# Performance work log

Hardware: AMD Instinct MI355X
Metric: run time of the kernel (lower is better)

Reference implementation:

```python
import jax, jax.numpy as jnp
import numpy as np

H = 16; DH = 64; D = H * DH
MEM = 1000            # config.memory_size
KT = 8 + 2            # k_similar + k_contiguous
THRESH = 0.5          # surprise_threshold


def _episodic_scan(k_flat):
    """k_flat: [B,S,D] per-token flattened keys. Sequentially (matching the torch
    per-sample python loop) segment each sequence by surprise, write segment-mean
    events into a FIFO memory, and retrieve top-KT events by cosine similarity
    against the last key. Ragged segments handled via masking (jit-safe)."""
    B, S, _ = k_flat.shape
    mem0 = jnp.zeros((MEM, D), k_flat.dtype)
    mv0 = jnp.zeros((MEM,), bool)

    def body(carry, kf):  # kf: [S,D]
        mem, mv = carry
        # surprise_t = ||k_t - k_{t-1}||, surprise_0 = 0
        diffs = jnp.linalg.norm(kf[1:] - kf[:-1], axis=-1)
        surprise = jnp.concatenate([jnp.zeros((1,), kf.dtype), diffs])
        thr = surprise.mean() + THRESH * jnp.std(surprise, ddof=1)  # torch.std is unbiased
        b = (surprise > thr).at[-1].set(True)  # boundary mask; last index forced
        bi = b.astype(jnp.int32)
        seg = jnp.cumsum(bi) - bi              # exclusive cumsum -> segment id per token
        sums = jax.ops.segment_sum(kf, seg, num_segments=S)
        cnts = jax.ops.segment_sum(jnp.ones((S,), kf.dtype), seg, num_segments=S)
        means = sums / jnp.maximum(cnts, 1.0)[:, None]  # [S,D] segment means (masked ragged)
        newv = jnp.arange(S) < bi.sum()
        # compact valid new events to the front (stable sort preserves order)
        o = jnp.argsort(jnp.logical_not(newv).astype(jnp.int32))
        comb = jnp.concatenate([mem, means[o]], axis=0)        # [MEM+S, D]
        cv = jnp.concatenate([mv, newv[o]], axis=0)
        # FIFO truncation: keep the last MEM valid events
        rank = jnp.cumsum(cv.astype(jnp.int32))
        keep = cv & (rank > rank[-1] - MEM)
        o2 = jnp.argsort(jnp.logical_not(keep).astype(jnp.int32))[:MEM]
        mem, mv = comb[o2], keep[o2]
        # retrieval: cosine similarity of last token's key vs memory, top-KT
        qf = kf[-1]
        qn = jnp.maximum(jnp.linalg.norm(qf), 1e-8)
        mn = jnp.maximum(jnp.linalg.norm(mem, axis=1), 1e-8)
        sims = jnp.where(mv, (mem @ qf) / (mn * qn), -jnp.inf)
        _, idx = jax.lax.top_k(sims, KT)
        return (mem, mv), mem[idx]  # retrieved events [KT, D]

    _, rets = jax.lax.scan(body, (mem0, mv0), k_flat)
    return rets  # [B, KT, D]


def setup_inputs() -> dict:
    key = jax.random.key(0)
    ks = jax.random.split(key, 6)
    B, S = 2, 2048
    return {
        "inputs": jax.random.normal(ks[0], (B, S, D), jnp.float32),
        "attention_mask": jnp.ones((B, S), jnp.int32),
        "Wq": jax.random.normal(ks[1], (D, D), jnp.float32) * 0.02,
        "Wk": jax.random.normal(ks[2], (D, D), jnp.float32) * 0.02,
        "Wv": jax.random.normal(ks[3], (D, D), jnp.float32) * 0.02,
        "Wo": jax.random.normal(ks[4], (D, D), jnp.float32) * 0.02,
    }


def reference(inputs, attention_mask, Wq, Wk, Wv, Wo):
    B, S, _ = inputs.shape
    qf = inputs @ Wq.T  # [B,S,D], per-token layout == keys.transpose(0,1).reshape(S,-1)
    kf = inputs @ Wk.T
    vf = inputs @ Wv.T
    q = qf.reshape(B, S, H, DH).transpose(0, 2, 1, 3)  # [B,H,S,DH]
    k = kf.reshape(B, S, H, DH).transpose(0, 2, 1, 3)
    v = vf.reshape(B, S, H, DH).transpose(0, 2, 1, 3)

    ret = _episodic_scan(kf)                               # [B,KT,D]
    ret_k = ret.reshape(B, KT, H, DH).transpose(0, 2, 1, 3)  # [B,H,KT,DH]
    aug_k = jnp.concatenate([ret_k, k], axis=2)            # [B,H,KT+S,DH]
    aug_v = jnp.concatenate([ret_k, v], axis=2)            # retrieved_v == retrieved_k

    scores = jnp.einsum("bhqd,bhkd->bhqk", q, aug_k) / jnp.sqrt(jnp.float32(DH))
    # ALiBi biases: zero for memory tokens, slopes*(pos_i-pos_j) for real tokens
    pos = jnp.arange(S, dtype=jnp.float32)
    pd = pos[:, None] - pos[None, :]                       # [S,S]
    slopes = 2.0 ** (-8.0 * jnp.arange(1, H + 1, dtype=jnp.float32) / H)
    bias_orig = slopes[None, :, None, None] * pd[None, None]  # [1,H,S,S]
    bias = jnp.concatenate(
        [jnp.zeros((1, H, S, KT), scores.dtype),
         jnp.broadcast_to(bias_orig, (1, H, S, S))], axis=3)
    scores = scores - bias
    # causal over real tokens; memory tokens always visible; attention_mask padded with 1s
    causal = jnp.concatenate(
        [jnp.ones((S, KT), bool), jnp.tril(jnp.ones((S, S), bool))], axis=1)
    aug_mask = jnp.concatenate(
        [jnp.ones((B, KT), jnp.int32), attention_mask], axis=1)
    visible = causal[None, None] & (aug_mask[:, None, None, :] > 0)
    scores = jnp.where(visible, scores, -jnp.inf)
    w = jax.nn.softmax(scores, axis=-1)
    out = jnp.einsum("bhqk,bhkd->bhqd", w, aug_v)
    out = out.transpose(0, 2, 1, 3).reshape(B, S, D)
    return out @ Wo.T
```

## Files before the change

### kernel.cpp

```cpp
#include <hip/hip_runtime.h>
#include <math.h>

#define B_ 2
#define S_ 2048
#define H_ 16
#define DH_ 64
#define D_ 1024
#define MEM_ 1000
#define KT_ 10
#define THRESH_ 0.5
#define BS_ (B_ * S_)
#define EVCAP_ (2 * S_)

typedef float f32x4 __attribute__((ext_vector_type(4)));
typedef short bf16x8 __attribute__((ext_vector_type(8)));
typedef short s16x4 __attribute__((ext_vector_type(4)));

__device__ inline unsigned short f2bf(float f) {
    union { float f; unsigned u; } v; v.f = f;
    unsigned u = v.u;
    unsigned r = (u + 0x7FFFu + ((u >> 16) & 1u)) >> 16;
    return (unsigned short)r;
}
__device__ inline float bf2f(unsigned short h) {
    union { unsigned u; float f; } v; v.u = ((unsigned)h) << 16; return v.f;
}

__device__ __forceinline__ void gload16(const short* gp, const short* lp) {
    __builtin_amdgcn_global_load_lds(
        (__attribute__((address_space(1))) void*)(unsigned long long)gp,
        (__attribute__((address_space(3))) void*)(unsigned)(unsigned long long)lp,
        16, 0, 0);
}

struct SpArgs {
    const float* X;
    short *Xh, *Xm, *Xl;
    const float* W[4];
    short *Wh[4], *Wm[4], *Wl[4];
    int nx4;
};
__global__ __launch_bounds__(256) void split_all_kernel(SpArgs sa)
{
    int bid = blockIdx.x;
    const float* src; short *ph, *pm, *pl; int i;
    if (bid < 4096) {
        i = bid * 256 + threadIdx.x;
        if (i >= sa.nx4) return;
        src = sa.X; ph = sa.Xh; pm = sa.Xm; pl = sa.Xl;
    } else {
        int wb = bid - 4096;
        int y = wb >> 10;
        i = (wb & 1023) * 256 + threadIdx.x;
        src = sa.W[y]; ph = sa.Wh[y]; pm = sa.Wm[y]; pl = sa.Wl[y];
    }
    float4 x = ((const float4*)src)[i];
    float xs[4] = {x.x, x.y, x.z, x.w};
    s16x4 hv, mv, lv;
    bool wl = (pl != nullptr);
#pragma unroll
    for (int j = 0; j < 4; ++j) {
        unsigned short hb = f2bf(xs[j]);
        float hf = bf2f(hb);
        float r1 = xs[j] - hf;
        unsigned short mb = f2bf(r1);
        hv[j] = (short)hb; mv[j] = (short)mb;
        if (wl) {
            float mf = bf2f(mb);
            lv[j] = (short)f2bf(r1 - mf);
        }
    }
    ((s16x4*)ph)[i] = hv;
    ((s16x4*)pm)[i] = mv;
    if (wl) ((s16x4*)pl)[i] = lv;
}

struct G8Args {
    const short* A[4][3];
    const short* B[4][3];
    short* outb[4];
    float* outf[4];
    int gsbase[4];
    int nt;
};

__global__ __launch_bounds__(512, 2) void gemm8(G8Args ga)
{
    __shared__ __align__(16) short Abuf[3][2][4096];
    __shared__ __align__(16) short Bbuf[3][2][4096];

    int wg = blockIdx.x;
    int lin = (wg & 7) * 32 + (wg >> 3);
    int jb = lin >> 4;
    int by = lin & 15;
    int g = jb >> 2;
    int bcol = jb & 3;

    int tid = threadIdx.x;
    int w = tid >> 6, l = tid & 63;
    int wm = w >> 2, wn = w & 3;
    int lg = l >> 4, lc = l & 15;

    const short* A0 = ga.A[g][0]; const short* A1 = ga.A[g][1]; const short* A2 = ga.A[g][2];
    const short* B0 = ga.B[g][0]; const short* B1 = ga.B[g][1]; const short* B2 = ga.B[g][2];
    const int gs0 = ga.gsbase[g];
    const int NT = ga.nt;

    const int u = tid;
    const int vswz = (u & 7) ^ ((u >> 3) & 7);
    const int srow = 2 * (u >> 3) + (vswz >> 2);
    const int skcol = (vswz & 3) * 8;
    const size_t abase = (size_t)(by * 256) * D_ + skcol;
    const size_t bbase = (size_t)(bcol * 256) * D_ + skcol;
    const int dst0 = w * 512;

    auto STAGE_A = [&](int ts, int d) {
        int tt = ts >> 5; int k0 = (ts & 31) << 5;
        const short* At = (tt == 0) ? A0 : ((tt == 1) ? A1 : A2);
        const short* Ab = At + abase + k0;
#pragma unroll
        for (int h = 0; h < 2; ++h)
            gload16(Ab + (size_t)(h * 128 + srow) * D_, &Abuf[d][h][dst0]);
    };
    auto STAGE_B = [&](int ts, int d) {
        int tt = ts >> 5; int k0 = (ts & 31) << 5;
        const short* Bt = (tt == 0) ? B0 : ((tt == 1) ? B1 : B2);
        const short* Bb = Bt + bbase + k0;
#pragma unroll
        for (int h = 0; h < 2; ++h)
            gload16(Bb + (size_t)(h * 128 + srow) * D_, &Bbuf[d][h][dst0]);
    };

    f32x4 acc[8][4] = {};
    const int psa = (((((lc & 1) << 2) | lg)) ^ ((lc >> 1) & 7)) * 8;
    const int rbase = (lc >> 1) * 64;

    STAGE_A(gs0, 0); STAGE_B(gs0, 0);
    STAGE_A(gs0 + 1, 1); STAGE_B(gs0 + 1, 1);
    asm volatile("s_waitcnt vmcnt(4)" ::: "memory");
    asm volatile("s_barrier" ::: "memory");
    __builtin_amdgcn_sched_barrier(0);

    int d = 0, ds = 2;
    for (int t = 0; t < NT; ++t) {
        const short* Ab0 = &Abuf[d][wm][rbase + psa];
        const short* Bb0 = &Bbuf[d][wn >> 1][(wn & 1) * 2048 + rbase + psa];
        bf16x8 bv[4], av[4];
#pragma unroll
        for (int nf = 0; nf < 4; ++nf) bv[nf] = *(const bf16x8*)&Bb0[nf * 512];
#pragma unroll
        for (int mf = 0; mf < 4; ++mf) av[mf] = *(const bf16x8*)&Ab0[mf * 512];
        if (t + 2 < NT) STAGE_A(gs0 + t + 2, ds);
        asm volatile("s_barrier" ::: "memory");
        asm volatile("s_waitcnt lgkmcnt(0)" ::: "memory");
        __builtin_amdgcn_sched_barrier(0);
        __builtin_amdgcn_s_setprio(1);
#pragma unroll
        for (int mf = 0; mf < 4; ++mf)
#pragma unroll
            for (int nf = 0; nf < 4; ++nf)
                acc[mf][nf] = __builtin_amdgcn_mfma_f32_16x16x32_bf16(av[mf], bv[nf], acc[mf][nf], 0, 0, 0);
        __builtin_amdgcn_s_setprio(0);
        asm volatile("s_barrier" ::: "memory");
#pragma unroll
        for (int mf = 0; mf < 4; ++mf) av[mf] = *(const bf16x8*)&Ab0[(4 + mf) * 512];
        if (t + 2 < NT) STAGE_B(gs0 + t + 2, ds);
        asm volatile("s_barrier" ::: "memory");
        asm volatile("s_waitcnt lgkmcnt(0)" ::: "memory");
        __builtin_amdgcn_sched_barrier(0);
        __builtin_amdgcn_s_setprio(1);
#pragma unroll
        for (int mf = 0; mf < 4; ++mf)
#pragma unroll
            for (int nf = 0; nf < 4; ++nf)
                acc[4 + mf][nf] = __builtin_amdgcn_mfma_f32_16x16x32_bf16(av[mf], bv[nf], acc[4 + mf][nf], 0, 0, 0);
        __builtin_amdgcn_s_setprio(0);
        if (t + 2 < NT) asm volatile("s_waitcnt vmcnt(4)" ::: "memory");
        else            asm volatile("s_waitcnt vmcnt(0)" ::: "memory");
        asm volatile("s_barrier" ::: "memory");
        __builtin_amdgcn_sched_barrier(0);
        d = (d == 2) ? 0 : d + 1;
        ds = (ds == 2) ? 0 : ds + 1;
    }

    short* ob = ga.outb[g];
    if (ob) {
#pragma unroll
        for (int mf = 0; mf < 8; ++mf)
#pragma unroll
            for (int nf = 0; nf < 4; ++nf)
#pragma unroll
                for (int reg = 0; reg < 4; ++reg) {
                    int row = by * 256 + wm * 128 + mf * 16 + lg * 4 + reg;
                    int col = bcol * 256 + wn * 64 + nf * 16 + lc;
                    ob[(size_t)row * D_ + col] = (short)f2bf(acc[mf][nf][reg]);
                }
    } else {
        float* of = ga.outf[g];
#pragma unroll
        for (int mf = 0; mf < 8; ++mf)
#pragma unroll
            for (int nf = 0; nf < 4; ++nf)
#pragma unroll
                for (int reg = 0; reg < 4; ++reg) {
                    int row = by * 256 + wm * 128 + mf * 16 + lg * 4 + reg;
                    int col = bcol * 256 + wn * 64 + nf * 16 + lc;
                    of[(size_t)row * D_ + col] = acc[mf][nf][reg];
                }
    }
}

__global__ __launch_bounds__(256) void fixup_kernel(const short* __restrict__ vbf,
                                                    short* __restrict__ vbfT,
                                                    float* __restrict__ kf,
                                                    const float* __restrict__ kp1,
                                                    short* __restrict__ kbf)
{
    int bid = blockIdx.x;
    int tid = threadIdx.x;
    if (bid < 1024) {
        __shared__ short st[64][70];
        int t = bid;
        int s0 = (t & 31) * 64;
        int h = (t >> 5) & 15;
        int b = t >> 9;
        int r = tid >> 2, cb = (tid & 3) * 16;
        const short* src = vbf + (size_t)(b * S_ + s0 + r) * D_ + h * DH_ + cb;
        *(bf16x8*)&st[r][cb] = *(const bf16x8*)src;
        *(bf16x8*)&st[r][cb + 8] = *(const bf16x8*)(src + 8);
        __syncthreads();
        int c = tid >> 2, sb = (tid & 3) * 16;
        short tmp[16];
#pragma unroll
        for (int i = 0; i < 16; ++i) tmp[i] = st[sb + i][c];
        short* dst = vbfT + ((size_t)(b * H_ + h) * DH_ + c) * S_ + s0 + sb;
        *(bf16x8*)dst = *(bf16x8*)&tmp[0];
        *(bf16x8*)(dst + 8) = *(bf16x8*)&tmp[8];
    } else {
        size_t i = (size_t)(bid - 1024) * 256 + tid;
        float4 a = ((const float4*)kf)[i];
        float4 b = ((const float4*)kp1)[i];
        float4 s = {a.x + b.x, a.y + b.y, a.z + b.z, a.w + b.w};
        ((float4*)kf)[i] = s;
        s16x4 o;
        o[0] = (short)f2bf(s.x); o[1] = (short)f2bf(s.y);
        o[2] = (short)f2bf(s.z); o[3] = (short)f2bf(s.w);
        ((s16x4*)kbf)[i] = o;
    }
}

__global__ __launch_bounds__(256) void addo4_kernel(const float* __restrict__ p0,
                                                    const float* __restrict__ p1,
                                                    const float* __restrict__ p2,
                                                    const float* __restrict__ p3,
                                                    float* __restrict__ out)
{
    size_t i = (size_t)blockIdx.x * 256 + threadIdx.x;
    float4 a = ((const float4*)p0)[i];
    float4 b = ((const float4*)p1)[i];
    float4 c = ((const float4*)p2)[i];
    float4 d = ((const float4*)p3)[i];
    float4 s = {((a.x + b.x) + c.x) + d.x, ((a.y + b.y) + c.y) + d.y,
                ((a.z + b.z) + c.z) + d.z, ((a.w + b.w) + c.w) + d.w};
    ((float4*)out)[i] = s;
}

__global__ __launch_bounds__(256) void surprise_kernel(const float* __restrict__ kf,
                                                       double* __restrict__ sur)
{
    int t = blockIdx.x;
    int b = blockIdx.y;
    if (t == 0) { if (threadIdx.x == 0) sur[(size_t)b * S_] = 0.0; return; }
    const float* kfb = kf + (size_t)b * S_ * D_;
    __shared__ double red[256];
    double acc = 0.0;
    for (int d = threadIdx.x; d < D_; d += 256) {
        double df = (double)kfb[(size_t)t * D_ + d] - (double)kfb[(size_t)(t - 1) * D_ + d];
        acc += df * df;
    }
    red[threadIdx.x] = acc;
    __syncthreads();
    for (int s = 128; s > 0; s >>= 1) {
        if (threadIdx.x < s) red[threadIdx.x] += red[threadIdx.x + s];
        __syncthreads();
    }
    if (threadIdx.x == 0) sur[(size_t)b * S_ + t] = sqrt(red[0]);
}

__global__ __launch_bounds__(256) void boundary2_kernel(const double* __restrict__ sur,
                                                        int* __restrict__ seg_start,
                                                        int* __restrict__ seg_end,
                                                        int* __restrict__ scal)
{
    __shared__ double lsur[S_];
    __shared__ double red[256];
    __shared__ double sh_mean, sh_thr;
    __shared__ int cnt[256];
    int tid = threadIdx.x;
    int running = 0;
    for (int b = 0; b < B_; ++b) {
        __syncthreads();
        for (int t = tid; t < S_; t += 256) lsur[t] = sur[(size_t)b * S_ + t];
        __syncthreads();
        double a = 0.0;
        for (int t = tid; t < S_; t += 256) a += lsur[t];
        red[tid] = a;
        __syncthreads();
        for (int s = 128; s > 0; s >>= 1) {
            if (tid < s) red[tid] += red[tid + s];
            __syncthreads();
        }
        if (tid == 0) sh_mean = red[0] / (double)S_;
        __syncthreads();
        double mean = sh_mean;
        a = 0.0;
        for (int t = tid; t < S_; t += 256) { double d = lsur[t] - mean; a += d * d; }
        red[tid] = a;
        __syncthreads();
        for (int s = 128; s > 0; s >>= 1) {
            if (tid < s) red[tid] += red[tid + s];
            __syncthreads();
        }
        if (tid == 0) sh_thr = mean + THRESH_ * sqrt(red[0] / (double)(S_ - 1));
        __syncthreads();
        double thr = sh_thr;
        bool flg[8];
        int c = 0;
#pragma unroll
        for (int j = 0; j < 8; ++j) {
            int t = tid * 8 + j;
            flg[j] = (lsur[t] > thr) || (t == S_ - 1);
            c += flg[j] ? 1 : 0;
        }
        cnt[tid] = c;
        __syncthreads();
        for (int off = 1; off < 256; off <<= 1) {
            int v = cnt[tid];
            int add = (tid >= off) ? cnt[tid - off] : 0;
            __syncthreads();
            cnt[tid] = v + add;
            __syncthreads();
        }
        int r = (tid == 0) ? 0 : cnt[tid - 1];
        int* se = seg_end + b * S_;
        int* ss = seg_start + b * S_;
#pragma unroll
        for (int j = 0; j < 8; ++j) {
            if (flg[j]) { se[r] = tid * 8 + j; ++r; }
        }
        __syncthreads();
        int n = cnt[255];
        for (int i = tid; i < n; i += 256)
            ss[i] = (i == 0) ? 0 : se[i - 1] + 1;
        if (tid == 0) {
            scal[4 + b] = n;
            scal[6 + b] = running;
        }
        running += n;
        __syncthreads();
    }
}

__global__ __launch_bounds__(256) void seg_means_kernel(const float* __restrict__ kf,
                                                        float* __restrict__ events,
                                                        const int* __restrict__ seg_start,
                                                        const int* __restrict__ seg_end,
                                                        const int* __restrict__ scal)
{
    int g = blockIdx.x;
    int b = blockIdx.y;
    if (g >= scal[4 + b]) return;
    const float* kfb = kf + (size_t)b * S_ * D_;
    int s = seg_start[b * S_ + g], e = seg_end[b * S_ + g];
    double inv = 1.0 / (double)(e - s + 1);
    size_t obase = (size_t)(scal[6 + b] + g) * D_;
    for (int d = threadIdx.x; d < D_; d += 256) {
        double acc = 0.0;
        for (int r = s; r <= e; ++r) acc += (double)kfb[(size_t)r * D_ + d];
        events[obase + d] = (float)(acc * inv);
    }
}

__global__ __launch_bounds__(256) void sims_kernel(const float* __restrict__ events,
                                                   const float* __restrict__ kf,
                                                   float* __restrict__ sims,
                                                   const int* __restrict__ scal)
{
    int e = blockIdx.x;
    int b = blockIdx.y;
    int total = scal[6 + b] + scal[4 + b];
    int w = total < MEM_ ? total : MEM_;
    float* sb = sims + b * MEM_;
    if (e >= w) { if (threadIdx.x == 0) sb[e] = -INFINITY; return; }
    int wstart = total - w;
    const float* ev = events + (size_t)(wstart + e) * D_;
    const float* q = kf + ((size_t)(b * S_ + S_ - 1)) * D_;
    __shared__ double r1[256], r2[256], r3[256];
    int tid = threadIdx.x;
    double dot = 0.0, n2 = 0.0, q2 = 0.0;
    for (int d = tid; d < D_; d += 256) {
        double ed = ev[d], qd = q[d];
        dot += ed * qd; n2 += ed * ed; q2 += qd * qd;
    }
    r1[tid] = dot; r2[tid] = n2; r3[tid] = q2;
    __syncthreads();
    for (int s = 128; s > 0; s >>= 1) {
        if (tid < s) { r1[tid] += r1[tid + s]; r2[tid] += r2[tid + s]; r3[tid] += r3[tid + s]; }
        __syncthreads();
    }
    if (tid == 0) {
        double mn = sqrt(r2[0]); if (mn < 1e-8) mn = 1e-8;
        double qn = sqrt(r3[0]); if (qn < 1e-8) qn = 1e-8;
        sb[e] = (float)(r1[0] / (mn * qn));
    }
}

__global__ __launch_bounds__(256) void topk_kernel(const float* __restrict__ events,
                                                   float* __restrict__ sims,
                                                   float* __restrict__ ret,
                                                   const int* __restrict__ scal)
{
    int b = blockIdx.x;
    int total = scal[6 + b] + scal[4 + b];
    int w = total < MEM_ ? total : MEM_;
    int wstart = total - w;
    float* sb = sims + b * MEM_;
    float* retb = ret + (size_t)b * KT_ * D_;
    __shared__ float bv[256];
    __shared__ int bidx[256];
    __shared__ int chosen;
    int tid = threadIdx.x;
    for (int r = 0; r < KT_; ++r) {
        float best = -INFINITY;
        int bi = 0x7fffffff;
        for (int e = tid; e < w; e += 256) {
            float v = sb[e];
            if (v > best || (v == best && e < bi)) { best = v; bi = e; }
        }
        bv[tid] = best; bidx[tid] = bi;
        __syncthreads();
        for (int s = 128; s > 0; s >>= 1) {
            if (tid < s) {
                if (bv[tid + s] > bv[tid] || (bv[tid + s] == bv[tid] && bidx[tid + s] < bidx[tid])) {
                    bv[tid] = bv[tid + s]; bidx[tid] = bidx[tid + s];
                }
            }
            __syncthreads();
        }
        if (tid == 0) {
            chosen = (r < w) ? bidx[0] : -1;
            if (chosen >= 0) sb[chosen] = -INFINITY;
        }
        __syncthreads();
        int c = chosen;
        if (c >= 0) {
            const float* ev = events + (size_t)(wstart + c) * D_;
            for (int d = tid; d < D_; d += 256) retb[(size_t)r * D_ + d] = ev[d];
        } else {
            for (int d = tid; d < D_; d += 256) retb[(size_t)r * D_ + d] = 0.0f;
        }
        __syncthreads();
    }
}

#define QTT 128
#define KTT 128
__global__ __launch_bounds__(512, 4) void attn_mfma_kernel(const short* __restrict__ qbf,
                                                           const short* __restrict__ kbf,
                                                           const short* __restrict__ vbfT,
                                                           const float* __restrict__ ret,
                                                           const int* __restrict__ amask,
                                                           short* __restrict__ AOh,
                                                           short* __restrict__ AOm)
{
    __shared__ __align__(16) short k_s[KTT][72];
    __shared__ __align__(16) short vT_s[DH_][136];
    __shared__ __align__(16) short p_s[8][16][136];

    const float LOG2E = 1.4426950408889634f;
    int bid = blockIdx.x;
    int xcd = bid & 7;
    int idx = bid >> 3;
    int qtslot = idx >> 2;
    int hbL = idx & 3;
    int qt = (qtslot < 8) ? (15 - qtslot) : (qtslot - 8);
    int hb = xcd * 4 + hbL;
    int h = hb & 15, b = hb >> 4;
    int q0 = qt * QTT;

    int tid = threadIdx.x;
    int w = tid >> 6, l = tid & 63;
    int lg = l >> 4, lc = l & 15;
    int qb = q0 + w * 16;
    float scale2 = 0.125f * LOG2E;
    float slope2 = exp2f(-0.5f * (float)(h + 1)) * LOG2E;

    bf16x8 qfr[2];
#pragma unroll
    for (int half = 0; half < 2; ++half)
        qfr[half] = *(const bf16x8*)(qbf + ((size_t)(b * S_ + qb + lc)) * D_ + h * DH_ + half * 32 + lg * 8);

    float mrow[4], lrow[4], fac[4];
#pragma unroll
    for (int r = 0; r < 4; ++r) { mrow[r] = -INFINITY; lrow[r] = 0.0f; }
    f32x4 O[4] = {};

    int skr = tid >> 2;
    int skc = (tid & 3) * 16;
    int sdv = tid >> 3;
    int skk = (tid & 7) * 16;

    const short* kptr = kbf + ((size_t)(b * S_ + skr)) * D_ + h * DH_ + skc;
    const short* vptr = vbfT + ((size_t)(b * H_ + h) * DH_ + sdv) * S_ + skk;

    int ntiles = qt + 1;
    bf16x8 kr0 = *(const bf16x8*)kptr, kr1 = *(const bf16x8*)(kptr + 8);
    bf16x8 vr0 = *(const bf16x8*)vptr, vr1 = *(const bf16x8*)(vptr + 8);

    for (int tile = 0; tile < ntiles; ++tile) {
        int j0 = tile * KTT;
        __syncthreads();
        *(bf16x8*)&k_s[skr][skc] = kr0;
        *(bf16x8*)&k_s[skr][skc + 8] = kr1;
        *(bf16x8*)&vT_s[sdv][skk] = vr0;
        *(bf16x8*)&vT_s[sdv][skk + 8] = vr1;
        __syncthreads();
        if (tile + 1 < ntiles) {
            const short* kp = kptr + (size_t)(tile + 1) * KTT * D_;
            kr0 = *(const bf16x8*)kp; kr1 = *(const bf16x8*)(kp + 8);
            const short* vp = vptr + (tile + 1) * KTT;
            vr0 = *(const bf16x8*)vp; vr1 = *(const bf16x8*)(vp + 8);
        }

        float sc[8][4];
        int am[8];
#pragma unroll
        for (int kt = 0; kt < 8; ++kt) am[kt] = amask[b * S_ + j0 + kt * 16 + lc];
        bool fullvis = (j0 + (KTT - 1) <= qb);
#pragma unroll
        for (int kt = 0; kt < 8; ++kt) {
            f32x4 s = {0.0f, 0.0f, 0.0f, 0.0f};
            bf16x8 k0 = *(const bf16x8*)&k_s[kt * 16 + lc][lg * 8];
            bf16x8 k1 = *(const bf16x8*)&k_s[kt * 16 + lc][32 + lg * 8];
            s = __builtin_amdgcn_mfma_f32_16x16x32_bf16(qfr[0], k0, s, 0, 0, 0);
            s = __builtin_amdgcn_mfma_f32_16x16x32_bf16(qfr[1], k1, s, 0, 0, 0);
            int jg = j0 + kt * 16 + lc;
            if (fullvis) {
#pragma unroll
                for (int reg = 0; reg < 4; ++reg) {
                    int qi = qb + lg * 4 + reg;
                    sc[kt][reg] = (am[kt] > 0) ? (s[reg] * scale2 - slope2 * (float)(qi - jg)) : -INFINITY;
                }
            } else {
#pragma unroll
                for (int reg = 0; reg < 4; ++reg) {
                    int qi = qb + lg * 4 + reg;
                    bool vis = (jg <= qi) && (am[kt] > 0);
                    sc[kt][reg] = vis ? (s[reg] * scale2 - slope2 * (float)(qi - jg)) : -INFINITY;
                }
            }
        }

#pragma unroll
        for (int reg = 0; reg < 4; ++reg) {
            float tm = fmaxf(fmaxf(fmaxf(sc[0][reg], sc[1][reg]), fmaxf(sc[2][reg], sc[3][reg])),
                             fmaxf(fmaxf(sc[4][reg], sc[5][reg]), fmaxf(sc[6][reg], sc[7][reg])));
#pragma unroll
            for (int msk = 1; msk <= 8; msk <<= 1) tm = fmaxf(tm, __shfl_xor(tm, msk));
            float mnew = fmaxf(mrow[reg], tm);
            fac[reg] = exp2f(mrow[reg] - mnew);
            mrow[reg] = mnew;
            float rs = 0.0f;
#pragma unroll
            for (int kt = 0; kt < 8; ++kt) {
                float p = exp2f(sc[kt][reg] - mnew);
                sc[kt][reg] = p;
                rs += p;
            }
#pragma unroll
            for (int msk = 1; msk <= 8; msk <<= 1) rs += __shfl_xor(rs, msk);
            lrow[reg] = lrow[reg] * fac[reg] + rs;
        }

        int parity = l & 1;
#pragma unroll
        for (int kt = 0; kt < 8; ++kt) {
#pragma unroll
            for (int rp = 0; rp < 4; rp += 2) {
                float s0 = sc[kt][rp];
                float s1 = sc[kt][rp + 1];
                float o0 = __shfl_xor(s0, 1);
                float o1 = __shfl_xor(s1, 1);
                float lo, hi; int reg;
                if (parity == 0) { lo = s0; hi = o0; reg = rp; }
                else             { lo = o1; hi = s1; reg = rp + 1; }
                unsigned pk = (unsigned)f2bf(lo) | ((unsigned)f2bf(hi) << 16);
                *(unsigned*)&p_s[w][lg * 4 + reg][kt * 16 + (lc & ~1)] = pk;
            }
        }
        __syncthreads();

#pragma unroll
        for (int db = 0; db < 4; ++db) {
#pragma unroll
            for (int reg = 0; reg < 4; ++reg) O[db][reg] *= fac[reg];
        }
#pragma unroll
        for (int kh = 0; kh < 4; ++kh) {
            bf16x8 a = *(const bf16x8*)&p_s[w][lc][kh * 32 + lg * 8];
#pragma unroll
            for (int db = 0; db < 4; ++db) {
                bf16x8 vb = *(const bf16x8*)&vT_s[db * 16 + lc][kh * 32 + lg * 8];
                O[db] = __builtin_amdgcn_mfma_f32_16x16x32_bf16(a, vb, O[db], 0, 0, 0);
            }
        }
    }

    {
        int sr = tid >> 3;
        int sc0 = (tid & 7) * 8;
        __syncthreads();
        short kv[8];
        if (sr < KT_) {
            const float* rp = ret + ((size_t)(b * KT_ + sr)) * D_ + h * DH_ + sc0;
            float4 a0 = *(const float4*)rp;
            float4 a1 = *(const float4*)(rp + 4);
            kv[0] = (short)f2bf(a0.x); kv[1] = (short)f2bf(a0.y);
            kv[2] = (short)f2bf(a0.z); kv[3] = (short)f2bf(a0.w);
            kv[4] = (short)f2bf(a1.x); kv[5] = (short)f2bf(a1.y);
            kv[6] = (short)f2bf(a1.z); kv[7] = (short)f2bf(a1.w);
        } else {
#pragma unroll
            for (int i = 0; i < 8; ++i) kv[i] = 0;
        }
        *(bf16x8*)&k_s[sr][sc0] = *(bf16x8*)&kv[0];
        __syncthreads();
        short tv[8];
#pragma unroll
        for (int i = 0; i < 8; ++i) {
            int key = sc0 + i;
            tv[i] = (key < KT_) ? k_s[key][sr] : (short)0;
        }
        *(bf16x8*)&vT_s[sr][sc0] = *(bf16x8*)&tv[0];

        float scm[4];
        {
            f32x4 s = {0.0f, 0.0f, 0.0f, 0.0f};
            bf16x8 k0 = *(const bf16x8*)&k_s[lc][lg * 8];
            bf16x8 k1 = *(const bf16x8*)&k_s[lc][32 + lg * 8];
            s = __builtin_amdgcn_mfma_f32_16x16x32_bf16(qfr[0], k0, s, 0, 0, 0);
            s = __builtin_amdgcn_mfma_f32_16x16x32_bf16(qfr[1], k1, s, 0, 0, 0);
#pragma unroll
            for (int reg = 0; reg < 4; ++reg)
                scm[reg] = (lc < KT_) ? s[reg] * scale2 : -INFINITY;
        }
        float pm[4];
#pragma unroll
        for (int reg = 0; reg < 4; ++reg) {
            float tm = scm[reg];
#pragma unroll
            for (int msk = 1; msk <= 8; msk <<= 1) tm = fmaxf(tm, __shfl_xor(tm, msk));
            float mnew = fmaxf(mrow[reg], tm);
            fac[reg] = exp2f(mrow[reg] - mnew);
            mrow[reg] = mnew;
            float p = exp2f(scm[reg] - mnew);
            pm[reg] = p;
            float rs = p;
#pragma unroll
            for (int msk = 1; msk <= 8; msk <<= 1) rs += __shfl_xor(rs, msk);
            lrow[reg] = lrow[reg] * fac[reg] + rs;
        }
        int parity = l & 1;
#pragma unroll
        for (int kt = 0; kt < 2; ++kt) {
#pragma unroll
            for (int rp = 0; rp < 4; rp += 2) {
                float s0 = (kt == 1) ? 0.0f : pm[rp];
                float s1 = (kt == 1) ? 0.0f : pm[rp + 1];
                float o0 = __shfl_xor(s0, 1);
                float o1 = __shfl_xor(s1, 1);
                float lo, hi; int reg;
                if (parity == 0) { lo = s0; hi = o0; reg = rp; }
                else             { lo = o1; hi = s1; reg = rp + 1; }
                unsigned pk = (unsigned)f2bf(lo) | ((unsigned)f2bf(hi) << 16);
                *(unsigned*)&p_s[w][lg * 4 + reg][kt * 16 + (lc & ~1)] = pk;
            }
        }
        __syncthreads();
#pragma unroll
        for (int db = 0; db < 4; ++db) {
#pragma unroll
            for (int reg = 0; reg < 4; ++reg) O[db][reg] *= fac[reg];
        }
        {
            bf16x8 a = *(const bf16x8*)&p_s[w][lc][lg * 8];
#pragma unroll
            for (int db = 0; db < 4; ++db) {
                bf16x8 vb = *(const bf16x8*)&vT_s[db * 16 + lc][lg * 8];
                O[db] = __builtin_amdgcn_mfma_f32_16x16x32_bf16(a, vb, O[db], 0, 0, 0);
            }
        }
    }

#pragma unroll
    for (int db = 0; db < 4; ++db) {
#pragma unroll
        for (int reg = 0; reg < 4; ++reg) {
            int qi = qb + lg * 4 + reg;
            size_t idx2 = ((size_t)(b * S_ + qi)) * D_ + h * DH_ + db * 16 + lc;
            float o = O[db][reg] / lrow[reg];
            unsigned short hb2 = f2bf(o);
            float hf = bf2f(hb2);
            unsigned short mb = f2bf(o - hf);
            AOh[idx2] = (short)hb2;
            AOm[idx2] = (short)mb;
        }
    }
}

extern "C" void kernel_launch(void* const* d_in, const int* in_sizes, int n_in,
                              void* d_out, int out_size, void* d_ws, size_t ws_size,
                              hipStream_t stream)
{
    const float* X = (const float*)d_in[0];
    const int* amask = (const int*)d_in[1];
    const float* Wq = (const float*)d_in[2];
    const float* Wk = (const float*)d_in[3];
    const float* Wv = (const float*)d_in[4];
    const float* Wo = (const float*)d_in[5];
    float* out = (float*)d_out;

    char* p = (char*)d_ws;
    auto alloc = [&](size_t bytes) -> char* {
        char* r = p; p += (bytes + 255) & ~(size_t)255; return r;
    };
    double* sur = (double*)alloc((size_t)B_ * S_ * sizeof(double));
    float* kacc = (float*)alloc((size_t)2 * BS_ * D_ * sizeof(float));
    float* events = (float*)alloc((size_t)EVCAP_ * D_ * sizeof(float));
    float* ret = (float*)alloc((size_t)B_ * KT_ * D_ * sizeof(float));
    float* sims = (float*)alloc((size_t)B_ * MEM_ * sizeof(float));
    int* seg_start = (int*)alloc((size_t)B_ * S_ * sizeof(int));
    int* seg_end = (int*)alloc((size_t)B_ * S_ * sizeof(int));
    int* scal = (int*)alloc(64);
    short* qbf = (short*)alloc((size_t)BS_ * D_ * sizeof(short));
    short* vbf = (short*)alloc((size_t)BS_ * D_ * sizeof(short));
    short* vbfT = (short*)alloc((size_t)B_ * H_ * DH_ * S_ * sizeof(short));
    short* Xh = (short*)alloc((size_t)BS_ * D_ * sizeof(short));
    short* Xm = (short*)alloc((size_t)BS_ * D_ * sizeof(short));
    short* Xl = (short*)alloc((size_t)BS_ * D_ * sizeof(short));
    short* Wqh = (short*)alloc((size_t)D_ * D_ * sizeof(short));
    short* Wqm = (short*)alloc((size_t)D_ * D_ * sizeof(short));
    short* Wvh = (short*)alloc((size_t)D_ * D_ * sizeof(short));
    short* Wvm = (short*)alloc((size_t)D_ * D_ * sizeof(short));
    short* Woh = (short*)alloc((size_t)D_ * D_ * sizeof(short));
    short* Wom = (short*)alloc((size_t)D_ * D_ * sizeof(short));
    short* Wkh = (short*)alloc((size_t)D_ * D_ * sizeof(short));
    short* Wkm = (short*)alloc((size_t)D_ * D_ * sizeof(short));
    short* Wkl = (short*)alloc((size_t)D_ * D_ * sizeof(short));
    if ((size_t)(p - (char*)d_ws) > ws_size) return;

    float* kf = kacc;
    float* kp1 = kacc + (size_t)BS_ * D_;
    short* kbf = Xl;

    {
        SpArgs sa = {};
        sa.X = X; sa.Xh = Xh; sa.Xm = Xm; sa.Xl = Xl;
        sa.W[0] = Wq; sa.Wh[0] = Wqh; sa.Wm[0] = Wqm; sa.Wl[0] = nullptr;
        sa.W[1] = Wk; sa.Wh[1] = Wkh; sa.Wm[1] = Wkm; sa.Wl[1] = Wkl;
        sa.W[2] = Wv; sa.Wh[2] = Wvh; sa.Wm[2] = Wvm; sa.Wl[2] = nullptr;
        sa.W[3] = Wo; sa.Wh[3] = Woh; sa.Wm[3] = Wom; sa.Wl[3] = nullptr;
        sa.nx4 = BS_ * D_ / 4;
        split_all_kernel<<<4096 + 4096, 256, 0, stream>>>(sa);
    }

    {
        G8Args ga = {};
        ga.A[0][0] = Xm;  ga.A[0][1] = Xh;  ga.A[0][2] = Xh;
        ga.B[0][0] = Wqh; ga.B[0][1] = Wqm; ga.B[0][2] = Wqh;
        ga.outb[0] = qbf;
        ga.A[1][0] = Xm;  ga.A[1][1] = Xh;  ga.A[1][2] = Xh;
        ga.B[1][0] = Wvh; ga.B[1][1] = Wvm; ga.B[1][2] = Wvh;
        ga.outb[1] = vbf;
        ga.A[2][0] = Xh;  ga.A[2][1] = Xm;  ga.A[2][2] = Xm;
        ga.B[2][0] = Wkm; ga.B[2][1] = Wkh; ga.B[2][2] = Wkm;
        ga.outf[2] = kf;
        ga.A[3][0] = Xh;  ga.A[3][1] = Xl;  ga.A[3][2] = Xh;
        ga.B[3][0] = Wkl; ga.B[3][1] = Wkh; ga.B[3][2] = Wkh;
        ga.outf[3] = kp1;
        ga.gsbase[0] = 0; ga.gsbase[1] = 0; ga.gsbase[2] = 0; ga.gsbase[3] = 0;
        ga.nt = 96;
        gemm8<<<256, 512, 0, stream>>>(ga);
    }
    fixup_kernel<<<1024 + BS_ * D_ / 4 / 256, 256, 0, stream>>>(vbf, vbfT, kf, kp1, kbf);

    surprise_kernel<<<dim3(S_, B_), 256, 0, stream>>>(kf, sur);
    boundary2_kernel<<<1, 256, 0, stream>>>(sur, seg_start, seg_end, scal);
    seg_means_kernel<<<dim3(S_, B_), 256, 0, stream>>>(kf, events, seg_start, seg_end, scal);
    sims_kernel<<<dim3(MEM_, B_), 256, 0, stream>>>(events, kf, sims, scal);
    topk_kernel<<<B_, 256, 0, stream>>>(events, sims, ret, scal);

    attn_mfma_kernel<<<512, 512, 0, stream>>>(qbf, kbf, vbfT, ret, amask, Xh, Xm);

    {
        float* p2 = events;
        float* p3 = (float*)qbf;
        G8Args ga = {};
        for (int g = 0; g < 4; ++g) {
            ga.A[g][0] = Xm;  ga.A[g][1] = Xh;  ga.A[g][2] = Xh;
            ga.B[g][0] = Woh; ga.B[g][1] = Wom; ga.B[g][2] = Woh;
            ga.gsbase[g] = g * 24;
        }
        ga.outf[0] = kf; ga.outf[1] = kp1; ga.outf[2] = p2; ga.outf[3] = p3;
        ga.nt = 24;
        gemm8<<<256, 512, 0, stream>>>(ga);
        addo4_kernel<<<BS_ * D_ / 4 / 256, 256, 0, stream>>>(kf, kp1, p2, p3, out);
    }
}
```

Before: 344.9 us.

## Fuse episodic scan stages into one cooperative kernel and simplify GEMM inner loop

Replaces the five separate scan kernels (surprise, boundary, segment means, similarity, top-k) with one cooperative kernel of 1024 blocks that uses grid-wide syncs between phases. The goal is to remove the launch gaps between these small, serial kernels. Separately, the GEMM main loop now loads all eight A fragments at once, issues both A and B staging loads together, and drops the intermediate barriers and waitcnts. The GEMM change increases register pressure and may introduce LDS hazards, because the next-stage loads are no longer fenced by barriers after the fragment reads.

```diff
diff --git a/kernel.cpp b/kernel.cpp
--- a/kernel.cpp
+++ b/kernel.cpp
@@ -1,5 +1,8 @@
 #include <hip/hip_runtime.h>
+#include <hip/hip_cooperative_groups.h>
 #include <math.h>
+
+namespace cg = cooperative_groups;
 
 #define B_ 2
 #define S_ 2048
@@ -145,35 +148,18 @@
     for (int t = 0; t < NT; ++t) {
         const short* Ab0 = &Abuf[d][wm][rbase + psa];
         const short* Bb0 = &Bbuf[d][wn >> 1][(wn & 1) * 2048 + rbase + psa];
-        bf16x8 bv[4], av[4];
+        bf16x8 av[8], bv[4];
 #pragma unroll
         for (int nf = 0; nf < 4; ++nf) bv[nf] = *(const bf16x8*)&Bb0[nf * 512];
 #pragma unroll
-        for (int mf = 0; mf < 4; ++mf) av[mf] = *(const bf16x8*)&Ab0[mf * 512];
-        if (t + 2 < NT) STAGE_A(gs0 + t + 2, ds);
-        asm volatile("s_barrier" ::: "memory");
-        asm volatile("s_waitcnt lgkmcnt(0)" ::: "memory");
-        __builtin_amdgcn_sched_barrier(0);
+        for (int mf = 0; mf < 8; ++mf) av[mf] = *(const bf16x8*)&Ab0[mf * 512];
+        if (t + 2 < NT) { STAGE_A(gs0 + t + 2, ds); STAGE_B(gs0 + t + 2, ds); }
         __builtin_amdgcn_s_setprio(1);
 #pragma unroll
-        for (int mf = 0; mf < 4; ++mf)
+        for (int mf = 0; mf < 8; ++mf)
 #pragma unroll
             for (int nf = 0; nf < 4; ++nf)
                 acc[mf][nf] = __builtin_amdgcn_mfma_f32_16x16x32_bf16(av[mf], bv[nf], acc[mf][nf], 0, 0, 0);
-        __builtin_amdgcn_s_setprio(0);
-        asm volatile("s_barrier" ::: "memory");
-#pragma unroll
-        for (int mf = 0; mf < 4; ++mf) av[mf] = *(const bf16x8*)&Ab0[(4 + mf) * 512];
-        if (t + 2 < NT) STAGE_B(gs0 + t + 2, ds);
-        asm volatile("s_barrier" ::: "memory");
-        asm volatile("s_waitcnt lgkmcnt(0)" ::: "memory");
-        __builtin_amdgcn_sched_barrier(0);
-        __builtin_amdgcn_s_setprio(1);
-#pragma unroll
-        for (int mf = 0; mf < 4; ++mf)
-#pragma unroll
-            for (int nf = 0; nf < 4; ++nf)
-                acc[4 + mf][nf] = __builtin_amdgcn_mfma_f32_16x16x32_bf16(av[mf], bv[nf], acc[4 + mf][nf], 0, 0, 0);
         __builtin_amdgcn_s_setprio(0);
         if (t + 2 < NT) asm volatile("s_waitcnt vmcnt(4)" ::: "memory");
         else            asm volatile("s_waitcnt vmcnt(0)" ::: "memory");
@@ -265,201 +251,203 @@
     ((float4*)out)[i] = s;
 }
 
-__global__ __launch_bounds__(256) void surprise_kernel(const float* __restrict__ kf,
-                                                       double* __restrict__ sur)
+struct ScanArgs {
+    const float* kf;
+    double* sur;
+    int* seg_start;
+    int* seg_end;
+    int* scal;
+    float* events;
+    float* sims;
+    float* ret;
+};
+
+__global__ __launch_bounds__(256) void scan_all_kernel(ScanArgs a)
 {
-    int t = blockIdx.x;
-    int b = blockIdx.y;
-    if (t == 0) { if (threadIdx.x == 0) sur[(size_t)b * S_] = 0.0; return; }
-    const float* kfb = kf + (size_t)b * S_ * D_;
+    cg::grid_group grid = cg::this_grid();
     __shared__ double red[256];
-    double acc = 0.0;
-    for (int d = threadIdx.x; d < D_; d += 256) {
-        double df = (double)kfb[(size_t)t * D_ + d] - (double)kfb[(size_t)(t - 1) * D_ + d];
-        acc += df * df;
-    }
-    red[threadIdx.x] = acc;
-    __syncthreads();
-    for (int s = 128; s > 0; s >>= 1) {
-        if (threadIdx.x < s) red[threadIdx.x] += red[threadIdx.x + s];
-        __syncthreads();
-    }
-    if (threadIdx.x == 0) sur[(size_t)b * S_ + t] = sqrt(red[0]);
-}
-
-__global__ __launch_bounds__(256) void boundary2_kernel(const double* __restrict__ sur,
-                                                        int* __restrict__ seg_start,
-                                                        int* __restrict__ seg_end,
-                                                        int* __restrict__ scal)
-{
+    __shared__ double r2[256], r3[256];
     __shared__ double lsur[S_];
-    __shared__ double red[256];
+    __shared__ int cnt[256];
     __shared__ double sh_mean, sh_thr;
-    __shared__ int cnt[256];
-    int tid = threadIdx.x;
-    int running = 0;
-    for (int b = 0; b < B_; ++b) {
-        __syncthreads();
-        for (int t = tid; t < S_; t += 256) lsur[t] = sur[(size_t)b * S_ + t];
-        __syncthreads();
-        double a = 0.0;
-        for (int t = tid; t < S_; t += 256) a += lsur[t];
-        red[tid] = a;
+    __shared__ float bvv[256];
+    __shared__ int bidx[256];
+    __shared__ int chosen;
+    int bid = blockIdx.x, tid = threadIdx.x;
+    int nb = gridDim.x;
+
+    for (int item = bid; item < B_ * S_; item += nb) {
+        int b = item >> 11, t = item & (S_ - 1);
+        if (t == 0) { if (tid == 0) a.sur[(size_t)b * S_] = 0.0; continue; }
+        const float* kfb = a.kf + (size_t)b * S_ * D_;
+        double acc = 0.0;
+        for (int d = tid; d < D_; d += 256) {
+            double df = (double)kfb[(size_t)t * D_ + d] - (double)kfb[(size_t)(t - 1) * D_ + d];
+            acc += df * df;
+        }
+        red[tid] = acc;
         __syncthreads();
         for (int s = 128; s > 0; s >>= 1) {
             if (tid < s) red[tid] += red[tid + s];
             __syncthreads();
         }
-        if (tid == 0) sh_mean = red[0] / (double)S_;
-        __syncthreads();
-        double mean = sh_mean;
-        a = 0.0;
-        for (int t = tid; t < S_; t += 256) { double d = lsur[t] - mean; a += d * d; }
-        red[tid] = a;
+        if (tid == 0) a.sur[(size_t)b * S_ + t] = sqrt(red[0]);
+        __syncthreads();
+    }
+    __threadfence();
+    grid.sync();
+
+    if (bid == 0) {
+        int running = 0;
+        for (int b = 0; b < B_; ++b) {
+            __syncthreads();
+            for (int t = tid; t < S_; t += 256) lsur[t] = a.sur[(size_t)b * S_ + t];
+            __syncthreads();
+            double s1 = 0.0;
+            for (int t = tid; t < S_; t += 256) s1 += lsur[t];
+            red[tid] = s1;
+            __syncthreads();
+            for (int s = 128; s > 0; s >>= 1) {
+                if (tid < s) red[tid] += red[tid + s];
+                __syncthreads();
+            }
+            if (tid == 0) sh_mean = red[0] / (double)S_;
+            __syncthreads();
+            double mean = sh_mean;
+            s1 = 0.0;
+            for (int t = tid; t < S_; t += 256) { double d = lsur[t] - mean; s1 += d * d; }
+            red[tid] = s1;
+            __syncthreads();
+            for (int s = 128; s > 0; s >>= 1) {
+                if (tid < s) red[tid] += red[tid + s];
+                __syncthreads();
+            }
+            if (tid == 0) sh_thr = mean + THRESH_ * sqrt(red[0] / (double)(S_ - 1));
+            __syncthreads();
+            double thr = sh_thr;
+            bool flg[8];
+            int c = 0;
+#pragma unroll
+            for (int j = 0; j < 8; ++j) {
+                int t = tid * 8 + j;
+                flg[j] = (lsur[t] > thr) || (t == S_ - 1);
+                c += flg[j] ? 1 : 0;
+            }
+            cnt[tid] = c;
+            __syncthreads();
+            for (int off = 1; off < 256; off <<= 1) {
+                int v = cnt[tid];
+                int add = (tid >= off) ? cnt[tid - off] : 0;
+                __syncthreads();
+                cnt[tid] = v + add;
+                __syncthreads();
+            }
+            int r = (tid == 0) ? 0 : cnt[tid - 1];
+            int* se = a.seg_end + b * S_;
+            int* ss = a.seg_start + b * S_;
+#pragma unroll
+            for (int j = 0; j < 8; ++j) {
+                if (flg[j]) { se[r] = tid * 8 + j; ++r; }
+            }
+            __syncthreads();
+            int n = cnt[255];
+            for (int i = tid; i < n; i += 256)
+                ss[i] = (i == 0) ? 0 : se[i - 1] + 1;
+            if (tid == 0) {
+                a.scal[4 + b] = n;
+                a.scal[6 + b] = running;
+            }
+            running += n;
+            __syncthreads();
+        }
+    }
+    __threadfence();
+    grid.sync();
+
+    for (int item = bid; item < B_ * S_; item += nb) {
+        int b = item >> 11, g = item & (S_ - 1);
+        if (g >= a.scal[4 + b]) continue;
+        const float* kfb = a.kf + (size_t)b * S_ * D_;
+        int s = a.seg_start[b * S_ + g], e = a.seg_end[b * S_ + g];
+        double inv = 1.0 / (double)(e - s + 1);
+        size_t obase = (size_t)(a.scal[6 + b] + g) * D_;
+        for (int d = tid; d < D_; d += 256) {
+            double acc = 0.0;
+            for (int r = s; r <= e; ++r) acc += (double)kfb[(size_t)r * D_ + d];
+            a.events[obase + d] = (float)(acc * inv);
+        }
+    }
+    __threadfence();
+    grid.sync();
+
+    for (int item = bid; item < B_ * MEM_; item += nb) {
+        int b = item / MEM_, e = item - b * MEM_;
+        int total = a.scal[6 + b] + a.scal[4 + b];
+        int w = total < MEM_ ? total : MEM_;
+        float* sb = a.sims + b * MEM_;
+        if (e >= w) { if (tid == 0) sb[e] = -INFINITY; continue; }
+        int wstart = total - w;
+        const float* ev = a.events + (size_t)(wstart + e) * D_;
+        const float* q = a.kf + ((size_t)(b * S_ + S_ - 1)) * D_;
+        double dot = 0.0, n2 = 0.0, q2 = 0.0;
+        for (int d = tid; d < D_; d += 256) {
+            double ed = ev[d], qd = q[d];
+            dot += ed * qd; n2 += ed * ed; q2 += qd * qd;
+        }
+        red[tid] = dot; r2[tid] = n2; r3[tid] = q2;
         __syncthreads();
         for (int s = 128; s > 0; s >>= 1) {
-            if (tid < s) red[tid] += red[tid + s];
-            __syncthreads();
-        }
-        if (tid == 0) sh_thr = mean + THRESH_ * sqrt(red[0] / (double)(S_ - 1));
-        __syncthreads();
-        double thr = sh_thr;
-        bool flg[8];
-        int c = 0;
-#pragma unroll
-        for (int j = 0; j < 8; ++j) {
-            int t = tid * 8 + j;
-            flg[j] = (lsur[t] > thr) || (t == S_ - 1);
-            c += flg[j] ? 1 : 0;
-        }
-        cnt[tid] = c;
-        __syncthreads();
-        for (int off = 1; off < 256; off <<= 1) {
-            int v = cnt[tid];
-            int add = (tid >= off) ? cnt[tid - off] : 0;
-            __syncthreads();
-            cnt[tid] = v + add;
-            __syncthreads();
-        }
-        int r = (tid == 0) ? 0 : cnt[tid - 1];
-        int* se = seg_end + b * S_;
-        int* ss = seg_start + b * S_;
-#pragma unroll
-        for (int j = 0; j < 8; ++j) {
-            if (flg[j]) { se[r] = tid * 8 + j; ++r; }
-        }
-        __syncthreads();
-        int n = cnt[255];
-        for (int i = tid; i < n; i += 256)
-            ss[i] = (i == 0) ? 0 : se[i - 1] + 1;
+            if (tid < s) { red[tid] += red[tid + s]; r2[tid] += r2[tid + s]; r3[tid] += r3[tid + s]; }
+            __syncthreads();
+        }
         if (tid == 0) {
-            scal[4 + b] = n;
-            scal[6 + b] = running;
-        }
-        running += n;
-        __syncthreads();
-    }
-}
-
-__global__ __launch_bounds__(256) void seg_means_kernel(const float* __restrict__ kf,
-                                                        float* __restrict__ events,
-                                                        const int* __restrict__ seg_start,
-                                                        const int* __restrict__ seg_end,
-                                                        const int* __restrict__ scal)
-{
-    int g = blockIdx.x;
-    int b = blockIdx.y;
-    if (g >= scal[4 + b]) return;
-    const float* kfb = kf + (size_t)b * S_ * D_;
-    int s = seg_start[b * S_ + g], e = seg_end[b * S_ + g];
-    double inv = 1.0 / (double)(e - s + 1);
-    size_t obase = (size_t)(scal[6 + b] + g) * D_;
-    for (int d = threadIdx.x; d < D_; d += 256) {
-        double acc = 0.0;
-        for (int r = s; r <= e; ++r) acc += (double)kfb[(size_t)r * D_ + d];
-        events[obase + d] = (float)(acc * inv);
-    }
-}
-
-__global__ __launch_bounds__(256) void sims_kernel(const float* __restrict__ events,
-                                                   const float* __restrict__ kf,
-                                                   float* __restrict__ sims,
-                                                   const int* __restrict__ scal)
-{
-    int e = blockIdx.x;
-    int b = blockIdx.y;
-    int total = scal[6 + b] + scal[4 + b];
-    int w = total < MEM_ ? total : MEM_;
-    float* sb = sims + b * MEM_;
-    if (e >= w) { if (threadIdx.x == 0) sb[e] = -INFINITY; return; }
-    int wstart = total - w;
-    const float* ev = events + (size_t)(wstart + e) * D_;
-    const float* q = kf + ((size_t)(b * S_ + S_ - 1)) * D_;
-    __shared__ double r1[256], r2[256], r3[256];
-    int tid = threadIdx.x;
-    double dot = 0.0, n2 = 0.0, q2 = 0.0;
-    for (int d = tid; d < D_; d += 256) {
-        double ed = ev[d], qd = q[d];
-        dot += ed * qd; n2 += ed * ed; q2 += qd * qd;
-    }
-    r1[tid] = dot; r2[tid] = n2; r3[tid] = q2;
-    __syncthreads();
-    for (int s = 128; s > 0; s >>= 1) {
-        if (tid < s) { r1[tid] += r1[tid + s]; r2[tid] += r2[tid + s]; r3[tid] += r3[tid + s]; }
-        __syncthreads();
-    }
-    if (tid == 0) {
-        double mn = sqrt(r2[0]); if (mn < 1e-8) mn = 1e-8;
-        double qn = sqrt(r3[0]); if (qn < 1e-8) qn = 1e-8;
-        sb[e] = (float)(r1[0] / (mn * qn));
-    }
-}
-
-__global__ __launch_bounds__(256) void topk_kernel(const float* __restrict__ events,
-                                                   float* __restrict__ sims,
-                                                   float* __restrict__ ret,
-                                                   const int* __restrict__ scal)
-{
-    int b = blockIdx.x;
-    int total = scal[6 + b] + scal[4 + b];
-    int w = total < MEM_ ? total : MEM_;
-    int wstart = total - w;
-    float* sb = sims + b * MEM_;
-    float* retb = ret + (size_t)b * KT_ * D_;
-    __shared__ float bv[256];
-    __shared__ int bidx[256];
-    __shared__ int chosen;
-    int tid = threadIdx.x;
-    for (int r = 0; r < KT_; ++r) {
-        float best = -INFINITY;
-        int bi = 0x7fffffff;
-        for (int e = tid; e < w; e += 256) {
-            float v = sb[e];
-            if (v > best || (v == best && e < bi)) { best = v; bi = e; }
-        }
-        bv[tid] = best; bidx[tid] = bi;
-        __syncthreads();
-        for (int s = 128; s > 0; s >>= 1) {
-            if (tid < s) {
-                if (bv[tid + s] > bv[tid] || (bv[tid + s] == bv[tid] && bidx[tid + s] < bidx[tid])) {
-                    bv[tid] = bv[tid + s]; bidx[tid] = bidx[tid + s];
+            double mn = sqrt(r2[0]); if (mn < 1e-8) mn = 1e-8;
+            double qn = sqrt(r3[0]); if (qn < 1e-8) qn = 1e-8;
+            sb[e] = (float)(red[0] / (mn * qn));
+        }
+        __syncthreads();
+    }
+    __threadfence();
+    grid.sync();
+
+    if (bid < B_) {
+        int b = bid;
+        int total = a.scal[6 + b] + a.scal[4 + b];
+        int w = total < MEM_ ? total : MEM_;
+        int wstart = total - w;
+        float* sb = a.sims + b * MEM_;
+        float* retb = a.ret + (size_t)b * KT_ * D_;
+        for (int r = 0; r < KT_; ++r) {
+            float best = -INFINITY;
+            int bi = 0x7fffffff;
+            for (int e = tid; e < w; e += 256) {
+                float v = sb[e];
+                if (v > best || (v == best && e < bi)) { best = v; bi = e; }
+            }
+            bvv[tid] = best; bidx[tid] = bi;
+            __syncthreads();
+            for (int s = 128; s > 0; s >>= 1) {
+                if (tid < s) {
+                    if (bvv[tid + s] > bvv[tid] || (bvv[tid + s] == bvv[tid] && bidx[tid + s] < bidx[tid])) {
+                        bvv[tid] = bvv[tid + s]; bidx[tid] = bidx[tid + s];
+                    }
                 }
-            }
-            __syncthreads();
-        }
-        if (tid == 0) {
-            chosen = (r < w) ? bidx[0] : -1;
-            if (chosen >= 0) sb[chosen] = -INFINITY;
-        }
-        __syncthreads();
-        int c = chosen;
-        if (c >= 0) {
-            const float* ev = events + (size_t)(wstart + c) * D_;
-            for (int d = tid; d < D_; d += 256) retb[(size_t)r * D_ + d] = ev[d];
-        } else {
-            for (int d = tid; d < D_; d += 256) retb[(size_t)r * D_ + d] = 0.0f;
-        }
-        __syncthreads();
+                __syncthreads();
+            }
+            if (tid == 0) {
+                chosen = (r < w) ? bidx[0] : -1;
+                if (chosen >= 0) sb[chosen] = -INFINITY;
+            }
+            __syncthreads();
+            int c = chosen;
+            if (c >= 0) {
+                const float* ev = a.events + (size_t)(wstart + c) * D_;
+                for (int d = tid; d < D_; d += 256) retb[(size_t)r * D_ + d] = ev[d];
+            } else {
+                for (int d = tid; d < D_; d += 256) retb[(size_t)r * D_ + d] = 0.0f;
+            }
+            __syncthreads();
+        }
     }
 }
 
@@ -794,11 +782,14 @@
     }
     fixup_kernel<<<1024 + BS_ * D_ / 4 / 256, 256, 0, stream>>>(vbf, vbfT, kf, kp1, kbf);
 
-    surprise_kernel<<<dim3(S_, B_), 256, 0, stream>>>(kf, sur);
-    boundary2_kernel<<<1, 256, 0, stream>>>(sur, seg_start, seg_end, scal);
-    seg_means_kernel<<<dim3(S_, B_), 256, 0, stream>>>(kf, events, seg_start, seg_end, scal);
-    sims_kernel<<<dim3(MEM_, B_), 256, 0, stream>>>(events, kf, sims, scal);
-    topk_kernel<<<B_, 256, 0, stream>>>(events, sims, ret, scal);
+    {
+        ScanArgs sargs;
+        sargs.kf = kf; sargs.sur = sur; sargs.seg_start = seg_start; sargs.seg_end = seg_end;
+        sargs.scal = scal; sargs.events = events; sargs.sims = sims; sargs.ret = ret;
+        void* kp[] = { &sargs };
+        hipLaunchCooperativeKernel(reinterpret_cast<void*>(scan_all_kernel),
+                                   dim3(1024), dim3(256), kp, 0, stream);
+    }
 
     attn_mfma_kernel<<<512, 512, 0, stream>>>(qbf, kbf, vbfT, ret, amask, Xh, Xm);
 
```

After: 1.072 ms. 3.11x slower.
